# Performance work log

Hardware: AMD Instinct MI355X
Metric: run time of the kernel (lower is better)

The kernel has to match this reference:

```python
import jax, jax.numpy as jnp
import numpy as np

K = 7  # median blur kernel size

def median_blur(x, k=K):
    # kornia.filters.median_blur: zero padding, gather kxk window per pixel,
    # torch.median -> lower median = sorted index (k*k-1)//2 (== k*k//2 for odd k*k)
    pad = k // 2
    B, C, H, W = x.shape
    xp = jnp.pad(x, ((0, 0), (0, 0), (pad, pad), (pad, pad)))
    # [B, C, k*k, H, W] patch tensor (same as kornia's unfold via binary-kernel conv)
    patches = jnp.stack(
        [xp[:, :, i:i + H, j:j + W] for i in range(k) for j in range(k)], axis=2
    )
    return jnp.sort(patches, axis=2)[:, :, (k * k) // 2]


def setup_inputs() -> dict:
    key = jax.random.key(0)
    k1, k2 = jax.random.split(key)
    image = jax.random.normal(k1, (16, 3, 256, 256), dtype=jnp.float32)
    cover_image = jax.random.normal(k2, (16, 3, 256, 256), dtype=jnp.float32)
    return {"image": image, "cover_image": cover_image}


def reference(image, cover_image):
    x = (image + 1.0) / 2.0          # [-1,1] -> [0,1]
    x = median_blur(x, K)            # 7x7 median filter (p=1.0, always applied)
    x = x * 2.0 - 1.0                # [0,1] -> [-1,1]
    return jnp.clip(x, -1.0, 1.0)
```

## Files before the change

kernel.cpp:

```cpp
#include <hip/hip_runtime.h>
#include <stdint.h>


#define IMG_H 256
#define IMG_W 256
#define RROWS 8
#define RUNS  (IMG_H / RROWS)

#define PERM(a,b,s) __builtin_amdgcn_perm((a),(b),(s))

struct Planes { uint32_t pL[7], pH[7]; };

__device__ __forceinline__ Planes transpose7(
    uint32_t L0, uint32_t L1, uint32_t L2, uint32_t L3, uint32_t L4, uint32_t L5, uint32_t L6,
    uint32_t H0, uint32_t H1, uint32_t H2, uint32_t H3, uint32_t H4, uint32_t H5, uint32_t H6)
{
    Planes P;
    {
        uint32_t za1 = PERM(L1, L0, 0x05010400u), zb1 = PERM(L1, L0, 0x07030602u);
        uint32_t za2 = PERM(L3, L2, 0x05010400u), zb2 = PERM(L3, L2, 0x07030602u);
        uint32_t za3 = PERM(L5, L4, 0x05010400u), zb3 = PERM(L5, L4, 0x07030602u);
        uint32_t za4 = PERM(0u, L6, 0x05010400u), zb4 = PERM(0u, L6, 0x07030602u);
        P.pL[0] = PERM(za2, za1, 0x05040100u);  P.pH[0] = PERM(za4, za3, 0x05040100u);
        P.pL[1] = PERM(za2, za1, 0x07060302u);  P.pH[1] = PERM(za4, za3, 0x07060302u);
        P.pL[2] = PERM(zb2, zb1, 0x05040100u);  P.pH[2] = PERM(zb4, zb3, 0x05040100u);
        P.pL[3] = PERM(zb2, zb1, 0x07060302u);  P.pH[3] = PERM(zb4, zb3, 0x07060302u);
    }
    {
        uint32_t za1 = PERM(H1, H0, 0x05010400u), zb1 = PERM(H1, H0, 0x07030602u);
        uint32_t za2 = PERM(H3, H2, 0x05010400u), zb2 = PERM(H3, H2, 0x07030602u);
        uint32_t za3 = PERM(H5, H4, 0x05010400u), zb3 = PERM(H5, H4, 0x07030602u);
        uint32_t za4 = PERM(0u, H6, 0x05010400u), zb4 = PERM(0u, H6, 0x07030602u);
        P.pL[4] = PERM(za2, za1, 0x05040100u);  P.pH[4] = PERM(za4, za3, 0x05040100u);
        P.pL[5] = PERM(za2, za1, 0x07060302u);  P.pH[5] = PERM(za4, za3, 0x07060302u);
        P.pL[6] = PERM(zb2, zb1, 0x05040100u);  P.pH[6] = PERM(zb4, zb3, 0x05040100u);
    }
    return P;
}

__global__ __launch_bounds__(256, 6)
void median7_kernel(const float* __restrict__ img, float* __restrict__ out) {
    const int x     = threadIdx.x;
    const int plane = blockIdx.x / RUNS;
    const int run   = blockIdx.x % RUNS;
    const int y0    = run * RROWS;

    const float* ip = img + (size_t)plane * (IMG_H * IMG_W);
    float*       op = out + (size_t)plane * (IMG_H * IMG_W);

    __shared__ unsigned long long VA[2][IMG_W + 6];
    __shared__ unsigned long long VB[2][IMG_W + 6];
    if (x < 3) {
        VA[0][x] = 0ULL; VA[1][x] = 0ULL; VB[0][x] = 0ULL; VB[1][x] = 0ULL;
        VA[0][IMG_W + 3 + x] = 0ULL; VA[1][IMG_W + 3 + x] = 0ULL;
        VB[0][IMG_W + 3 + x] = 0ULL; VB[1][IMG_W + 3 + x] = 0ULL;
    }

    uint32_t vlo = 0u, vhi = 0u;

    auto insert = [&](int ry) {
        int rc = min(max(ry, 0), IMG_H - 1);
        float v = ip[rc * IMG_W + x];
        float t = fmaf(v, 63.5f, 64.0f);
        t = fminf(fmaxf(t, 0.0f), 127.0f);
        uint32_t q = (uint32_t)t;
        q = ((uint32_t)ry < (uint32_t)IMG_H) ? q : 0u;
        uint32_t nlo = ((q & 15u) * 0x08102040u) & 0x40404040u;
        uint32_t nhi = ((q >> 4)  * 0x08102040u) & 0x40404040u;
        vlo = ((vlo >> 1) & 0x3F3F3F3Fu) | nlo;
        vhi = ((vhi >> 1) & 0x3F3F3F3Fu) | nhi;
    };

#pragma unroll
    for (int j = 0; j < 6; ++j) insert(y0 - 3 + j);

#pragma unroll
    for (int rr = 0; rr < RROWS; rr += 2) {
        const int buf = (rr >> 1) & 1;

        insert(y0 + 3 + rr);
        const uint32_t alo = vlo, ahi = vhi;
        VA[buf][3 + x] = ((unsigned long long)ahi << 32) | alo;
        insert(y0 + 4 + rr);
        VB[buf][3 + x] = ((unsigned long long)vhi << 32) | vlo;
        __syncthreads();

        const unsigned long long* qa = &VA[buf][x];
        const unsigned long long* qb = &VB[buf][x];
        unsigned long long a0 = qa[0], a1 = qa[1], a2 = qa[2];
        unsigned long long a4 = qa[4], a5 = qa[5], a6 = qa[6];
        unsigned long long b0 = qb[0], b1 = qb[1], b2 = qb[2];
        unsigned long long b4 = qb[4], b5 = qb[5], b6 = qb[6];

        Planes PA = transpose7(
            (uint32_t)a0, (uint32_t)a1, (uint32_t)a2, alo,
            (uint32_t)a4, (uint32_t)a5, (uint32_t)a6,
            (uint32_t)(a0 >> 32), (uint32_t)(a1 >> 32), (uint32_t)(a2 >> 32), ahi,
            (uint32_t)(a4 >> 32), (uint32_t)(a5 >> 32), (uint32_t)(a6 >> 32));
        Planes PB = transpose7(
            (uint32_t)b0, (uint32_t)b1, (uint32_t)b2, vlo,
            (uint32_t)b4, (uint32_t)b5, (uint32_t)b6,
            (uint32_t)(b0 >> 32), (uint32_t)(b1 >> 32), (uint32_t)(b2 >> 32), vhi,
            (uint32_t)(b4 >> 32), (uint32_t)(b5 >> 32), (uint32_t)(b6 >> 32));

        uint32_t acloA = 0x7F7F7F7Fu, achiA = 0x007F7F7Fu, kA = 25u, medA = 0u;
        uint32_t acloB = 0x7F7F7F7Fu, achiB = 0x007F7F7Fu, kB = 25u, medB = 0u;
#pragma unroll
        for (int p = 6; p >= 0; --p) {
            {
                uint32_t ol = acloA & PA.pL[p], oh = achiA & PA.pH[p];
                uint32_t c1 = (uint32_t)(__popc(ol) + __popc(oh));
                bool b = (kA <= c1);
                acloA = b ? ol : (acloA ^ ol);
                achiA = b ? oh : (achiA ^ oh);
                kA    = b ? kA : (kA - c1);
                medA  = (medA << 1) | (b ? 1u : 0u);
            }
            {
                uint32_t ol = acloB & PB.pL[p], oh = achiB & PB.pH[p];
                uint32_t c1 = (uint32_t)(__popc(ol) + __popc(oh));
                bool b = (kB <= c1);
                acloB = b ? ol : (acloB ^ ol);
                achiB = b ? oh : (achiB ^ oh);
                kB    = b ? kB : (kB - c1);
                medB  = (medB << 1) | (b ? 1u : 0u);
            }
        }

        __builtin_nontemporal_store(fmaf((float)medA, 2.0f / 127.0f, -1.0f),
                                    &op[(y0 + rr) * IMG_W + x]);
        __builtin_nontemporal_store(fmaf((float)medB, 2.0f / 127.0f, -1.0f),
                                    &op[(y0 + rr + 1) * IMG_W + x]);
    }
}

extern "C" void kernel_launch(void* const* d_in, const int* in_sizes, int n_in,
                              void* d_out, int out_size, void* d_ws, size_t ws_size,
                              hipStream_t stream) {
    const float* img = (const float*)d_in[0];
    float* out = (float*)d_out;
    const int planes = in_sizes[0] / (IMG_H * IMG_W);
    dim3 grid(planes * RUNS);
    dim3 block(256);
    median7_kernel<<<grid, block, 0, stream>>>(img, out);
}
```

Before: 17.74 us.

## Software-pipeline row loads and merge shared buffers into 128-bit entries

The two row-pair shared arrays are merged into one ulonglong2 array, so each neighbour read becomes a single 128-bit LDS access instead of two 64-bit ones. Global loads for the next row pair are issued a step ahead, and the next step's insert and LDS store run before the current step's median computation. This is meant to hide global load latency behind the bit-sliced selection. In exchange, each iteration now ends with a barrier and a few more registers hold prefetched values, which may affect occupancy under the 6-wave launch bound.

After: 17.77 us. Within noise of the previous version (+0.2%).

```diff
diff --git a/kernel.cpp b/kernel.cpp
--- a/kernel.cpp
+++ b/kernel.cpp
@@ -48,19 +48,20 @@
     const float* ip = img + (size_t)plane * (IMG_H * IMG_W);
     float*       op = out + (size_t)plane * (IMG_H * IMG_W);
 
-    __shared__ unsigned long long VA[2][IMG_W + 6];
-    __shared__ unsigned long long VB[2][IMG_W + 6];
+    __shared__ ulonglong2 VL[2][IMG_W + 6];
     if (x < 3) {
-        VA[0][x] = 0ULL; VA[1][x] = 0ULL; VB[0][x] = 0ULL; VB[1][x] = 0ULL;
-        VA[0][IMG_W + 3 + x] = 0ULL; VA[1][IMG_W + 3 + x] = 0ULL;
-        VB[0][IMG_W + 3 + x] = 0ULL; VB[1][IMG_W + 3 + x] = 0ULL;
+        const ulonglong2 z = make_ulonglong2(0ULL, 0ULL);
+        VL[0][x] = z; VL[1][x] = z;
+        VL[0][IMG_W + 3 + x] = z; VL[1][IMG_W + 3 + x] = z;
     }
 
     uint32_t vlo = 0u, vhi = 0u;
 
-    auto insert = [&](int ry) {
+    auto loadrow = [&](int ry) -> float {
         int rc = min(max(ry, 0), IMG_H - 1);
-        float v = ip[rc * IMG_W + x];
+        return ip[rc * IMG_W + x];
+    };
+    auto insert_v = [&](float v, int ry) {
         float t = fmaf(v, 63.5f, 64.0f);
         t = fminf(fmaxf(t, 0.0f), 127.0f);
         uint32_t q = (uint32_t)t;
@@ -72,36 +73,47 @@
     };
 
 #pragma unroll
-    for (int j = 0; j < 6; ++j) insert(y0 - 3 + j);
+    for (int j = 0; j < 6; ++j) insert_v(loadrow(y0 - 3 + j), y0 - 3 + j);
+    insert_v(loadrow(y0 + 3), y0 + 3);
+    uint32_t palo = vlo, pahi = vhi;
+    insert_v(loadrow(y0 + 4), y0 + 4);
+    uint32_t pblo = vlo, pbhi = vhi;
+    VL[0][3 + x] = make_ulonglong2(((unsigned long long)pahi << 32) | palo,
+                                   ((unsigned long long)pbhi << 32) | pblo);
+    float f0 = loadrow(y0 + 5), f1 = loadrow(y0 + 6);
+    __syncthreads();
 
 #pragma unroll
-    for (int rr = 0; rr < RROWS; rr += 2) {
-        const int buf = (rr >> 1) & 1;
+    for (int i = 0; i < RROWS / 2; ++i) {
+        const int buf = i & 1;
 
-        insert(y0 + 3 + rr);
-        const uint32_t alo = vlo, ahi = vhi;
-        VA[buf][3 + x] = ((unsigned long long)ahi << 32) | alo;
-        insert(y0 + 4 + rr);
-        VB[buf][3 + x] = ((unsigned long long)vhi << 32) | vlo;
-        __syncthreads();
+        const ulonglong2* qp = &VL[buf][x];
+        ulonglong2 n0 = qp[0], n1 = qp[1], n2 = qp[2];
+        ulonglong2 n4 = qp[4], n5 = qp[5], n6 = qp[6];
 
-        const unsigned long long* qa = &VA[buf][x];
-        const unsigned long long* qb = &VB[buf][x];
-        unsigned long long a0 = qa[0], a1 = qa[1], a2 = qa[2];
-        unsigned long long a4 = qa[4], a5 = qa[5], a6 = qa[6];
-        unsigned long long b0 = qb[0], b1 = qb[1], b2 = qb[2];
-        unsigned long long b4 = qb[4], b5 = qb[5], b6 = qb[6];
+        const uint32_t calo = palo, cahi = pahi, cblo = pblo, cbhi = pbhi;
+
+        if (i < 3) {
+            insert_v(f0, y0 + 5 + 2 * i);
+            palo = vlo; pahi = vhi;
+            insert_v(f1, y0 + 6 + 2 * i);
+            pblo = vlo; pbhi = vhi;
+            VL[buf ^ 1][3 + x] =
+                make_ulonglong2(((unsigned long long)pahi << 32) | palo,
+                                ((unsigned long long)pbhi << 32) | pblo);
+        }
+        if (i < 2) { f0 = loadrow(y0 + 7 + 2 * i); f1 = loadrow(y0 + 8 + 2 * i); }
 
         Planes PA = transpose7(
-            (uint32_t)a0, (uint32_t)a1, (uint32_t)a2, alo,
-            (uint32_t)a4, (uint32_t)a5, (uint32_t)a6,
-            (uint32_t)(a0 >> 32), (uint32_t)(a1 >> 32), (uint32_t)(a2 >> 32), ahi,
-            (uint32_t)(a4 >> 32), (uint32_t)(a5 >> 32), (uint32_t)(a6 >> 32));
+            (uint32_t)n0.x, (uint32_t)n1.x, (uint32_t)n2.x, calo,
+            (uint32_t)n4.x, (uint32_t)n5.x, (uint32_t)n6.x,
+            (uint32_t)(n0.x >> 32), (uint32_t)(n1.x >> 32), (uint32_t)(n2.x >> 32), cahi,
+            (uint32_t)(n4.x >> 32), (uint32_t)(n5.x >> 32), (uint32_t)(n6.x >> 32));
         Planes PB = transpose7(
-            (uint32_t)b0, (uint32_t)b1, (uint32_t)b2, vlo,
-            (uint32_t)b4, (uint32_t)b5, (uint32_t)b6,
-            (uint32_t)(b0 >> 32), (uint32_t)(b1 >> 32), (uint32_t)(b2 >> 32), vhi,
-            (uint32_t)(b4 >> 32), (uint32_t)(b5 >> 32), (uint32_t)(b6 >> 32));
+            (uint32_t)n0.y, (uint32_t)n1.y, (uint32_t)n2.y, cblo,
+            (uint32_t)n4.y, (uint32_t)n5.y, (uint32_t)n6.y,
+            (uint32_t)(n0.y >> 32), (uint32_t)(n1.y >> 32), (uint32_t)(n2.y >> 32), cbhi,
+            (uint32_t)(n4.y >> 32), (uint32_t)(n5.y >> 32), (uint32_t)(n6.y >> 32));
 
         uint32_t acloA = 0x7F7F7F7Fu, achiA = 0x007F7F7Fu, kA = 25u, medA = 0u;
         uint32_t acloB = 0x7F7F7F7Fu, achiB = 0x007F7F7Fu, kB = 25u, medB = 0u;
@@ -128,9 +140,11 @@
         }
 
         __builtin_nontemporal_store(fmaf((float)medA, 2.0f / 127.0f, -1.0f),
-                                    &op[(y0 + rr) * IMG_W + x]);
+                                    &op[(y0 + 2 * i) * IMG_W + x]);
         __builtin_nontemporal_store(fmaf((float)medB, 2.0f / 127.0f, -1.0f),
-                                    &op[(y0 + rr + 1) * IMG_W + x]);
+                                    &op[(y0 + 2 * i + 1) * IMG_W + x]);
+
+        __syncthreads();
     }
 }
 
```

## Share one 8-row column window across two output rows, halve rows per block

Applied to the files above, without the earlier changes.

The vertical bitmask window now holds 8 rows instead of 7. One transposed plane set then serves two adjacent output rows: the upper 7 bits give one row and the lower 7 bits give the next, selected by different masks. This halves the shared-memory stores, transposes and LDS reads per output pair and removes the second VB buffer. It also halves RROWS to 4 so the grid has more blocks, raises the launch-bounds occupancy target to 8, and issues the global loads early. The cost is more halo-row reloading per block and possible register pressure at the higher occupancy target.

New measurement: 17.57 us. About the same (-0.9%).

```diff
diff --git a/kernel.cpp b/kernel.cpp
--- a/kernel.cpp
+++ b/kernel.cpp
@@ -4,16 +4,19 @@
 
 #define IMG_H 256
 #define IMG_W 256
-#define RROWS 8
+#define RROWS 4
 #define RUNS  (IMG_H / RROWS)
+typedef unsigned long long u64;
 
 #define PERM(a,b,s) __builtin_amdgcn_perm((a),(b),(s))
 
 struct Planes { uint32_t pL[7], pH[7]; };
 
 __device__ __forceinline__ Planes transpose7(
-    uint32_t L0, uint32_t L1, uint32_t L2, uint32_t L3, uint32_t L4, uint32_t L5, uint32_t L6,
-    uint32_t H0, uint32_t H1, uint32_t H2, uint32_t H3, uint32_t H4, uint32_t H5, uint32_t H6)
+    uint32_t L0, uint32_t L1, uint32_t L2, uint32_t L3,
+    uint32_t L4, uint32_t L5, uint32_t L6,
+    uint32_t H0, uint32_t H1, uint32_t H2, uint32_t H3,
+    uint32_t H4, uint32_t H5, uint32_t H6)
 {
     Planes P;
     {
@@ -38,99 +41,124 @@
     return P;
 }
 
-__global__ __launch_bounds__(256, 6)
+__device__ __forceinline__ uint32_t quant7(float v) {
+    float t = fmaf(v, 63.5f, 64.0f);
+    t = fminf(fmaxf(t, 0.0f), 127.0f);
+    return (uint32_t)t;
+}
+
+__device__ __forceinline__ void roll8(uint32_t& lo, uint32_t& hi, uint32_t q) {
+    uint32_t nlo = ((q & 15u) * 0x10204080u) & 0x80808080u;
+    uint32_t nhi = ((q >> 4)  * 0x10204080u) & 0x00808080u;
+    lo = ((lo >> 1) & 0x7F7F7F7Fu) | nlo;
+    hi = ((hi >> 1) & 0x007F7F7Fu) | nhi;
+}
+
+__device__ __forceinline__ void select2_store(
+    const Planes& P, float* __restrict__ op, int yA, int x)
+{
+    uint32_t acloA = 0x7F7F7F7Fu, achiA = 0x007F7F7Fu, kA = 25u, medA = 0u;
+    uint32_t acloB = 0xFEFEFEFEu, achiB = 0x00FEFEFEu, kB = 25u, medB = 0u;
+#pragma unroll
+    for (int p = 6; p >= 0; --p) {
+        {
+            uint32_t ol = acloA & P.pL[p], oh = achiA & P.pH[p];
+            uint32_t c1 = (uint32_t)(__popc(ol) + __popc(oh));
+            bool b = (kA <= c1);
+            acloA = b ? ol : (acloA ^ ol);
+            achiA = b ? oh : (achiA ^ oh);
+            kA    = b ? kA : (kA - c1);
+            medA  = (medA << 1) | (b ? 1u : 0u);
+        }
+        {
+            uint32_t ol = acloB & P.pL[p], oh = achiB & P.pH[p];
+            uint32_t c1 = (uint32_t)(__popc(ol) + __popc(oh));
+            bool b = (kB <= c1);
+            acloB = b ? ol : (acloB ^ ol);
+            achiB = b ? oh : (achiB ^ oh);
+            kB    = b ? kB : (kB - c1);
+            medB  = (medB << 1) | (b ? 1u : 0u);
+        }
+    }
+    __builtin_nontemporal_store(fmaf((float)medA, 2.0f / 127.0f, -1.0f),
+                                &op[yA * IMG_W + x]);
+    __builtin_nontemporal_store(fmaf((float)medB, 2.0f / 127.0f, -1.0f),
+                                &op[(yA + 1) * IMG_W + x]);
+}
+
+__global__ __launch_bounds__(256, 8)
 void median7_kernel(const float* __restrict__ img, float* __restrict__ out) {
-    const int x     = threadIdx.x;
-    const int plane = blockIdx.x / RUNS;
-    const int run   = blockIdx.x % RUNS;
-    const int y0    = run * RROWS;
+    const int x   = threadIdx.x;
+    const int pl  = blockIdx.x / RUNS;
+    const int run = blockIdx.x % RUNS;
+    const int y0  = run * RROWS;
 
-    const float* ip = img + (size_t)plane * (IMG_H * IMG_W);
-    float*       op = out + (size_t)plane * (IMG_H * IMG_W);
+    const float* ip = img + (size_t)pl * (IMG_H * IMG_W);
+    float*       op = out + (size_t)pl * (IMG_H * IMG_W);
 
-    __shared__ unsigned long long VA[2][IMG_W + 6];
-    __shared__ unsigned long long VB[2][IMG_W + 6];
+    __shared__ u64 VL[2][IMG_W + 6];
     if (x < 3) {
-        VA[0][x] = 0ULL; VA[1][x] = 0ULL; VB[0][x] = 0ULL; VB[1][x] = 0ULL;
-        VA[0][IMG_W + 3 + x] = 0ULL; VA[1][IMG_W + 3 + x] = 0ULL;
-        VB[0][IMG_W + 3 + x] = 0ULL; VB[1][IMG_W + 3 + x] = 0ULL;
+        VL[0][x] = 0ULL; VL[1][x] = 0ULL;
+        VL[0][IMG_W + 3 + x] = 0ULL; VL[1][IMG_W + 3 + x] = 0ULL;
     }
 
     uint32_t vlo = 0u, vhi = 0u;
 
-    auto insert = [&](int ry) {
-        int rc = min(max(ry, 0), IMG_H - 1);
-        float v = ip[rc * IMG_W + x];
-        float t = fmaf(v, 63.5f, 64.0f);
-        t = fminf(fmaxf(t, 0.0f), 127.0f);
-        uint32_t q = (uint32_t)t;
-        q = ((uint32_t)ry < (uint32_t)IMG_H) ? q : 0u;
-        uint32_t nlo = ((q & 15u) * 0x08102040u) & 0x40404040u;
-        uint32_t nhi = ((q >> 4)  * 0x08102040u) & 0x40404040u;
-        vlo = ((vlo >> 1) & 0x3F3F3F3Fu) | nlo;
-        vhi = ((vhi >> 1) & 0x3F3F3F3Fu) | nhi;
-    };
+    {
+        float pv[6];
+#pragma unroll
+        for (int j = 0; j < 6; ++j) {
+            int rc = max(y0 - 3 + j, 0);
+            pv[j] = ip[rc * IMG_W + x];
+        }
+#pragma unroll
+        for (int j = 0; j < 6; ++j) {
+            bool rok = (y0 - 3 + j) >= 0;
+            roll8(vlo, vhi, rok ? quant7(pv[j]) : 0u);
+        }
+    }
 
-#pragma unroll
-    for (int j = 0; j < 6; ++j) insert(y0 - 3 + j);
+    {
+        const int ry0 = y0 + 3, ry1 = y0 + 4;
+        float f0 = ip[min(ry0, IMG_H - 1) * IMG_W + x];
+        float f1 = ip[min(ry1, IMG_H - 1) * IMG_W + x];
+        roll8(vlo, vhi, (ry0 < IMG_H) ? quant7(f0) : 0u);
+        roll8(vlo, vhi, (ry1 < IMG_H) ? quant7(f1) : 0u);
+    }
+    VL[0][3 + x] = ((u64)vhi << 32) | vlo;
 
-#pragma unroll
-    for (int rr = 0; rr < RROWS; rr += 2) {
-        const int buf = (rr >> 1) & 1;
+    const int ry2 = y0 + 5, ry3 = y0 + 6;
+    float f2 = ip[min(ry2, IMG_H - 1) * IMG_W + x];
+    float f3 = ip[min(ry3, IMG_H - 1) * IMG_W + x];
 
-        insert(y0 + 3 + rr);
-        const uint32_t alo = vlo, ahi = vhi;
-        VA[buf][3 + x] = ((unsigned long long)ahi << 32) | alo;
-        insert(y0 + 4 + rr);
-        VB[buf][3 + x] = ((unsigned long long)vhi << 32) | vlo;
-        __syncthreads();
+    __syncthreads();
 
-        const unsigned long long* qa = &VA[buf][x];
-        const unsigned long long* qb = &VB[buf][x];
-        unsigned long long a0 = qa[0], a1 = qa[1], a2 = qa[2];
-        unsigned long long a4 = qa[4], a5 = qa[5], a6 = qa[6];
-        unsigned long long b0 = qb[0], b1 = qb[1], b2 = qb[2];
-        unsigned long long b4 = qb[4], b5 = qb[5], b6 = qb[6];
+    {
+        const u64* q = &VL[0][x];
+        u64 n0 = q[0], n1 = q[1], n2 = q[2], n4 = q[4], n5 = q[5], n6 = q[6];
+        Planes P = transpose7(
+            (uint32_t)n0, (uint32_t)n1, (uint32_t)n2, vlo,
+            (uint32_t)n4, (uint32_t)n5, (uint32_t)n6,
+            (uint32_t)(n0 >> 32), (uint32_t)(n1 >> 32), (uint32_t)(n2 >> 32), vhi,
+            (uint32_t)(n4 >> 32), (uint32_t)(n5 >> 32), (uint32_t)(n6 >> 32));
+        select2_store(P, op, y0, x);
+    }
 
-        Planes PA = transpose7(
-            (uint32_t)a0, (uint32_t)a1, (uint32_t)a2, alo,
-            (uint32_t)a4, (uint32_t)a5, (uint32_t)a6,
-            (uint32_t)(a0 >> 32), (uint32_t)(a1 >> 32), (uint32_t)(a2 >> 32), ahi,
-            (uint32_t)(a4 >> 32), (uint32_t)(a5 >> 32), (uint32_t)(a6 >> 32));
-        Planes PB = transpose7(
-            (uint32_t)b0, (uint32_t)b1, (uint32_t)b2, vlo,
-            (uint32_t)b4, (uint32_t)b5, (uint32_t)b6,
-            (uint32_t)(b0 >> 32), (uint32_t)(b1 >> 32), (uint32_t)(b2 >> 32), vhi,
-            (uint32_t)(b4 >> 32), (uint32_t)(b5 >> 32), (uint32_t)(b6 >> 32));
+    roll8(vlo, vhi, (ry2 < IMG_H) ? quant7(f2) : 0u);
+    roll8(vlo, vhi, (ry3 < IMG_H) ? quant7(f3) : 0u);
+    VL[1][3 + x] = ((u64)vhi << 32) | vlo;
 
-        uint32_t acloA = 0x7F7F7F7Fu, achiA = 0x007F7F7Fu, kA = 25u, medA = 0u;
-        uint32_t acloB = 0x7F7F7F7Fu, achiB = 0x007F7F7Fu, kB = 25u, medB = 0u;
-#pragma unroll
-        for (int p = 6; p >= 0; --p) {
-            {
-                uint32_t ol = acloA & PA.pL[p], oh = achiA & PA.pH[p];
-                uint32_t c1 = (uint32_t)(__popc(ol) + __popc(oh));
-                bool b = (kA <= c1);
-                acloA = b ? ol : (acloA ^ ol);
-                achiA = b ? oh : (achiA ^ oh);
-                kA    = b ? kA : (kA - c1);
-                medA  = (medA << 1) | (b ? 1u : 0u);
-            }
-            {
-                uint32_t ol = acloB & PB.pL[p], oh = achiB & PB.pH[p];
-                uint32_t c1 = (uint32_t)(__popc(ol) + __popc(oh));
-                bool b = (kB <= c1);
-                acloB = b ? ol : (acloB ^ ol);
-                achiB = b ? oh : (achiB ^ oh);
-                kB    = b ? kB : (kB - c1);
-                medB  = (medB << 1) | (b ? 1u : 0u);
-            }
-        }
+    __syncthreads();
 
-        __builtin_nontemporal_store(fmaf((float)medA, 2.0f / 127.0f, -1.0f),
-                                    &op[(y0 + rr) * IMG_W + x]);
-        __builtin_nontemporal_store(fmaf((float)medB, 2.0f / 127.0f, -1.0f),
-                                    &op[(y0 + rr + 1) * IMG_W + x]);
+    {
+        const u64* q = &VL[1][x];
+        u64 n0 = q[0], n1 = q[1], n2 = q[2], n4 = q[4], n5 = q[5], n6 = q[6];
+        Planes P = transpose7(
+            (uint32_t)n0, (uint32_t)n1, (uint32_t)n2, vlo,
+            (uint32_t)n4, (uint32_t)n5, (uint32_t)n6,
+            (uint32_t)(n0 >> 32), (uint32_t)(n1 >> 32), (uint32_t)(n2 >> 32), vhi,
+            (uint32_t)(n4 >> 32), (uint32_t)(n5 >> 32), (uint32_t)(n6 >> 32));
+        select2_store(P, op, y0 + 2, x);
     }
 }
 
```
